# Kernel tuning notes

Hardware: AMD Instinct MI355X
Metric: run time of the kernel (lower is better)

## Reference

```python
import jax, jax.numpy as jnp
import numpy as np

EPS = 1e-12  # matches torch F.normalize eps


def _l2norm(x, axis):
    n = jnp.sqrt(jnp.sum(x * x, axis=axis, keepdims=True))
    return x / jnp.maximum(n, EPS)


def setup_inputs() -> dict:
    key = jax.random.key(0)
    ks = jax.random.split(key, 12)
    B, C, H, W = 64, 2048, 14, 14
    hs, k = 1024, 512

    def xavier(kk, shape):
        fan_out, fan_in = shape[0], shape[1]
        a = float(np.sqrt(6.0 / (fan_in + fan_out)))
        return jax.random.uniform(kk, shape, jnp.float32, -a, a)

    return {
        "img": jax.random.normal(ks[0], (B, C, H, W), jnp.float32),
        "h": jax.random.normal(ks[1], (B, hs), jnp.float32),
        "wc": xavier(ks[2], (k, 1)),
        "bc": xavier(ks[3], (k, 1)),
        "whc": xavier(ks[4], (k, hs)),
        "wci": xavier(ks[5], (1, k)),
        "bci": xavier(ks[6], (1, 1)),
        "ws": xavier(ks[7], (k, C)),
        "bs": xavier(ks[8], (k, 1)),
        "whs": xavier(ks[9], (k, hs)),
        "wsi": xavier(ks[10], (1, k)),
        "bsi": xavier(ks[11], (1, 1)),
    }


def reference(img, h, wc, bc, whc, wci, bci, ws, bs, whs, wsi, bsi):
    B, C, H, W = img.shape
    P = H * W
    x = img.reshape(B, C, P)

    # ---- channel attention ----
    xc = _l2norm(x, axis=2)                      # normalize each channel over spatial
    ic = jnp.mean(xc, axis=2)                    # avgpool over HW -> [B, C]
    # wc [k,1] @ ic[:,None,:] [B,1,C] is a rank-1 outer product -> [B,k,C]
    t = jnp.tanh(wc[None, :, :] * ic[:, None, :] + bc[None, :, :]
                 + jnp.einsum('kh,bh->bk', whc, h)[:, :, None])  # [B,k,C]
    sc = jnp.einsum('k,bkc->bc', wci[0], t) + bci[0, 0]
    ac = jax.nn.softmax(sc, axis=1)              # [B, C]
    xw = x * ac[:, :, None]                      # channel-weighted features [B,C,P]

    # ---- spatial attention ----
    xs = _l2norm(xw, axis=1)                     # normalize each position over channels
    st = jnp.tanh(jnp.einsum('kc,bcp->bkp', ws, xs) + bs[None, :, :]
                  + jnp.einsum('kh,bh->bk', whs, h)[:, :, None])  # [B,k,P]
    ss = jnp.einsum('k,bkp->bp', wsi[0], st) + bsi[0, 0]
    asp = jax.nn.softmax(ss, axis=1)             # [B, P]
    out = xw * asp[:, None, :]                   # [B,C,P]
    return out.reshape(B, C, H, W)
```

## Files before the change

### kernel.cpp

```cpp
#include <hip/hip_runtime.h>

typedef unsigned short u16;
typedef short bf16x8 __attribute__((ext_vector_type(8)));
typedef float f32x4 __attribute__((ext_vector_type(4)));
typedef unsigned short u16x8 __attribute__((ext_vector_type(8)));

#define B_DIM 64
#define C_DIM 2048
#define P_DIM 196
#define K_DIM 512
#define HS_DIM 1024

static __device__ __forceinline__ u16 f2bf(float f) {
    union { float f; unsigned u; } v; v.f = f;
    unsigned r = v.u + 0x7FFF + ((v.u >> 16) & 1);
    return (u16)(r >> 16);
}

static __device__ __forceinline__ float fast_tanh(float a) {
    float e = __expf(2.f * a);
    return 1.f - 2.f / (e + 1.f);
}

__global__ void k1_rowstats(const float* __restrict__ x, float* __restrict__ ic) {
    int row = blockIdx.x * 4 + (threadIdx.x >> 6);
    int l = threadIdx.x & 63;
    const float* r = x + (size_t)row * P_DIM;
    float a0 = r[l], a1 = r[64 + l], a2 = r[128 + l];
    float a3 = (l < 4) ? r[192 + l] : 0.f;
    float s = a0 + a1 + a2 + a3;
    float q = a0 * a0 + a1 * a1 + a2 * a2 + a3 * a3;
    for (int off = 32; off; off >>= 1) { s += __shfl_down(s, off); q += __shfl_down(q, off); }
    if (l == 0) {
        float n = fmaxf(sqrtf(q), 1e-12f);
        ic[row] = s / ((float)P_DIM * n);
    }
}

__global__ __launch_bounds__(256) void k2_hproj(
    const float* __restrict__ h, const float* __restrict__ whc,
    const float* __restrict__ bc, const float* __restrict__ whs,
    const float* __restrict__ bs, float* __restrict__ u, float* __restrict__ v) {
    __shared__ float rc[1024], rs[1024];
    int k = blockIdx.x;
    int t = threadIdx.x, w = t >> 6, l = t & 63;
    for (int i = t; i < 1024; i += 256) {
        rc[i] = whc[(size_t)k * HS_DIM + i];
        rs[i] = whs[(size_t)k * HS_DIM + i];
    }
    __syncthreads();
    float bcv = bc[k], bsv = bs[k];
    for (int bb = 0; bb < 16; ++bb) {
        int b = (w << 4) + bb;
        const float* hr = h + (size_t)b * HS_DIM;
        float su = 0.f, sv = 0.f;
        #pragma unroll
        for (int j = 0; j < 16; ++j) {
            float hv = hr[l + (j << 6)];
            su = fmaf(rc[l + (j << 6)], hv, su);
            sv = fmaf(rs[l + (j << 6)], hv, sv);
        }
        #pragma unroll
        for (int off = 32; off; off >>= 1) { su += __shfl_down(su, off); sv += __shfl_down(sv, off); }
        if (l == 0) { u[b * K_DIM + k] = su + bcv; v[b * K_DIM + k] = sv + bsv; }
    }
}

__global__ void k2b_conv(const float* __restrict__ ws, u16* __restrict__ wsb2) {
    int i = blockIdx.x * 256 + threadIdx.x;
    int lane = i & 63;
    int kb = (i >> 6) & 31;
    int cstep = i >> 11;
    int r = kb * 16 + (lane & 15);
    int c0 = (cstep << 5) + ((lane >> 4) << 3);
    const float* src = ws + (size_t)r * C_DIM + c0;
    float4 f0 = *(const float4*)(src);
    float4 f1 = *(const float4*)(src + 4);
    u16x8 o;
    o[0] = f2bf(f0.x); o[1] = f2bf(f0.y); o[2] = f2bf(f0.z); o[3] = f2bf(f0.w);
    o[4] = f2bf(f1.x); o[5] = f2bf(f1.y); o[6] = f2bf(f1.z); o[7] = f2bf(f1.w);
    *(u16x8*)(wsb2 + (size_t)i * 8) = o;
}

__global__ void k3_sc(const float* __restrict__ ic, const float* __restrict__ u,
                      const float* __restrict__ wc, const float* __restrict__ wci,
                      const float* __restrict__ bci, float* __restrict__ sc) {
    __shared__ float swc[512], swci[512], su[512];
    int b = blockIdx.y;
    int c = blockIdx.x * 256 + threadIdx.x;
    for (int i = threadIdx.x; i < 512; i += 256) {
        swc[i] = wc[i]; swci[i] = wci[i]; su[i] = u[b * 512 + i];
    }
    __syncthreads();
    float icv = ic[(size_t)b * C_DIM + c];
    float s = 0.f;
    #pragma unroll 8
    for (int k = 0; k < 512; k++) {
        float a = fmaf(swc[k], icv, su[k]);
        s = fmaf(swci[k], fast_tanh(a), s);
    }
    sc[(size_t)b * C_DIM + c] = s + bci[0];
}

__global__ void k4_softmax_c(const float* __restrict__ sc, float* __restrict__ ac) {
    int b = blockIdx.x, t = threadIdx.x;
    __shared__ float red[4], red2[4];
    const float* s = sc + (size_t)b * C_DIM;
    float vals[8]; float m = -1e30f;
    #pragma unroll
    for (int i = 0; i < 8; i++) { vals[i] = s[t + i * 256]; m = fmaxf(m, vals[i]); }
    for (int off = 32; off; off >>= 1) m = fmaxf(m, __shfl_xor(m, off));
    if ((t & 63) == 0) red[t >> 6] = m;
    __syncthreads();
    m = fmaxf(fmaxf(red[0], red[1]), fmaxf(red[2], red[3]));
    float sum = 0.f;
    #pragma unroll
    for (int i = 0; i < 8; i++) { vals[i] = __expf(vals[i] - m); sum += vals[i]; }
    for (int off = 32; off; off >>= 1) sum += __shfl_xor(sum, off);
    if ((t & 63) == 0) red2[t >> 6] = sum;
    __syncthreads();
    sum = red2[0] + red2[1] + red2[2] + red2[3];
    float inv = 1.f / sum;
    float* a = ac + (size_t)b * C_DIM;
    #pragma unroll
    for (int i = 0; i < 8; i++) a[t + i * 256] = vals[i] * inv;
}

__global__ __launch_bounds__(256, 2) void k5_gemm(
    const float* __restrict__ x, const u16* __restrict__ wsb2,
    const float* __restrict__ ac, const float* __restrict__ vv,
    const float* __restrict__ wsi, float* __restrict__ ssp) {
    __shared__ __align__(16) u16 lB[2][64 * 32];
    __shared__ float lred[256];
    __shared__ float lcn[64];
    __shared__ float lss[4][64];

    const int p0 = blockIdx.x * 64;
    const int Rb = blockIdx.y * 256;
    const int b  = blockIdx.z;
    const int t = threadIdx.x;
    const int w = t >> 6, l = t & 63;
    const int lr16 = l & 15, lh = l >> 4;
    const int pg = l;
    const int co = w << 3;
    const int pp = p0 + pg;
    const bool pvld = pp < P_DIM;
    const int sBw = (pg >> 1) & 3;

    f32x4 acc[4][4];
    #pragma unroll
    for (int i = 0; i < 4; i++)
        #pragma unroll
        for (int j = 0; j < 4; j++)
            acc[i][j] = (f32x4){0.f, 0.f, 0.f, 0.f};

    float psum = 0.f;
    const float* xcol = x + (size_t)b * (C_DIM * P_DIM) + pp;
    const float* acrow = ac + (size_t)b * C_DIM;
    const bf16x8* abase = (const bf16x8*)wsb2 + ((Rb >> 4) + (w << 2)) * 64 + l;

    float xv[2][8], av[2][8];
    bf16x8 af[4][4];

    auto LOADX = [&](int step, int xs) {
        const int cc = (step << 5) + co;
        #pragma unroll
        for (int j = 0; j < 8; ++j)
            xv[xs][j] = pvld ? xcol[(size_t)(cc + j) * P_DIM] : 0.f;
        float4 a0 = *(const float4*)(acrow + cc);
        float4 a1 = *(const float4*)(acrow + cc + 4);
        av[xs][0] = a0.x; av[xs][1] = a0.y; av[xs][2] = a0.z; av[xs][3] = a0.w;
        av[xs][4] = a1.x; av[xs][5] = a1.y; av[xs][6] = a1.z; av[xs][7] = a1.w;
    };
    auto LOADA = [&](int step, int as_) {
        const bf16x8* p = abase + (size_t)step * 2048;
        #pragma unroll
        for (int mt = 0; mt < 4; ++mt) af[as_][mt] = p[mt * 64];
    };
    auto PROCB = [&](int xs, int bufi) {
        u16x8 pk;
        #pragma unroll
        for (int j = 0; j < 8; ++j) {
            float xw = xv[xs][j] * av[xs][j];
            psum = fmaf(xw, xw, psum);
            pk[j] = f2bf(xw);
        }
        *(u16x8*)&lB[bufi][(pg << 5) + ((w ^ sBw) << 3)] = pk;
    };
    auto RD_B = [&](int bufi, bf16x8* bfr) {
        #pragma unroll
        for (int nt = 0; nt < 4; ++nt) {
            int r = (nt << 4) + lr16;
            int s = (r >> 1) & 3;
            bfr[nt] = *(const bf16x8*)&lB[bufi][(r << 5) + ((lh ^ s) << 3)];
        }
    };
    auto MFMA16 = [&](int as_, const bf16x8* bfr) {
        __builtin_amdgcn_s_setprio(1);
        #pragma unroll
        for (int mt = 0; mt < 4; ++mt)
            #pragma unroll
            for (int nt = 0; nt < 4; ++nt)
                acc[mt][nt] = __builtin_amdgcn_mfma_f32_16x16x32_bf16(
                    af[as_][mt], bfr[nt], acc[mt][nt], 0, 0, 0);
        __builtin_amdgcn_s_setprio(0);
    };

    LOADX(0, 0); LOADA(0, 0);
    LOADX(1, 1); LOADA(1, 1);
    PROCB(0, 0);
    asm volatile("s_waitcnt lgkmcnt(0)" ::: "memory");
    __builtin_amdgcn_s_barrier();

    for (int ii = 0; ii < 15; ++ii) {
        const int base = ii << 2;
        #pragma unroll
        for (int S = 0; S < 4; ++S) {
            bf16x8 bfr[4];
            RD_B(S & 1, bfr);
            LOADX(base + S + 2, S & 1);
            LOADA(base + S + 2, (S + 2) & 3);
            MFMA16(S & 3, bfr);
            PROCB((S + 1) & 1, (S + 1) & 1);
            asm volatile("s_waitcnt lgkmcnt(0)" ::: "memory");
            __builtin_amdgcn_s_barrier();
        }
    }
    #pragma unroll
    for (int S = 0; S < 4; ++S) {
        bf16x8 bfr[4];
        RD_B(S & 1, bfr);
        if (S < 2) { LOADX(62 + S, S & 1); LOADA(62 + S, (S + 2) & 3); }
        MFMA16(S & 3, bfr);
        if (S < 3) PROCB((S + 1) & 1, (S + 1) & 1);
        asm volatile("s_waitcnt lgkmcnt(0)" ::: "memory");
        __builtin_amdgcn_s_barrier();
    }

    lred[t] = psum;
    __syncthreads();
    if (t < 64) {
        float cs = lred[t] + lred[t + 64] + lred[t + 128] + lred[t + 192];
        lcn[t] = fmaxf(sqrtf(cs), 1e-12f);
    }
    __syncthreads();

    float ssv[4] = {0.f, 0.f, 0.f, 0.f};
    #pragma unroll
    for (int mt = 0; mt < 4; ++mt) {
        int rl = (w << 6) + (mt << 4) + (lh << 2);
        #pragma unroll
        for (int j = 0; j < 4; ++j) {
            int r = Rb + rl + j;
            float wsiv = wsi[r];
            float vb = vv[b * K_DIM + r];
            #pragma unroll
            for (int nt = 0; nt < 4; ++nt) {
                float cn = lcn[(nt << 4) + lr16];
                float a = acc[mt][nt][j] / cn + vb;
                ssv[nt] = fmaf(wsiv, fast_tanh(a), ssv[nt]);
            }
        }
    }
    #pragma unroll
    for (int nt = 0; nt < 4; ++nt) {
        ssv[nt] += __shfl_xor(ssv[nt], 16);
        ssv[nt] += __shfl_xor(ssv[nt], 32);
    }
    if (lh == 0) {
        #pragma unroll
        for (int nt = 0; nt < 4; ++nt) lss[w][(nt << 4) + lr16] = ssv[nt];
    }
    __syncthreads();
    if (t < 64) {
        float s = lss[0][t] + lss[1][t] + lss[2][t] + lss[3][t];
        ssp[((blockIdx.y << 6) + b) * 256 + p0 + t] = s;
    }
}

__global__ void k6_softmax_p(const float* __restrict__ ssp, const float* __restrict__ bsi,
                             float* __restrict__ asp) {
    int b = blockIdx.x, t = threadIdx.x;
    __shared__ float red[4], red2[4];
    float val = -1e30f;
    if (t < P_DIM) val = ssp[b * 256 + t] + ssp[(64 + b) * 256 + t] + bsi[0];
    float m = val;
    for (int off = 32; off; off >>= 1) m = fmaxf(m, __shfl_xor(m, off));
    if ((t & 63) == 0) red[t >> 6] = m;
    __syncthreads();
    m = fmaxf(fmaxf(red[0], red[1]), fmaxf(red[2], red[3]));
    float e = (t < P_DIM) ? __expf(val - m) : 0.f;
    float sum = e;
    for (int off = 32; off; off >>= 1) sum += __shfl_xor(sum, off);
    if ((t & 63) == 0) red2[t >> 6] = sum;
    __syncthreads();
    sum = red2[0] + red2[1] + red2[2] + red2[3];
    if (t < P_DIM) asp[b * P_DIM + t] = e / sum;
}

__global__ void k7_out(const float* __restrict__ x, const float* __restrict__ ac,
                       const float* __restrict__ asp, float* __restrict__ out) {
    int idx = blockIdx.x * 256 + threadIdx.x;
    int row = idx / 49;
    int pq = idx - row * 49;
    int b = row >> 11;
    float a = ac[row];
    float4 xv = ((const float4*)x)[idx];
    float4 pv = *(const float4*)&asp[b * P_DIM + pq * 4];
    float4 o;
    o.x = xv.x * a * pv.x;
    o.y = xv.y * a * pv.y;
    o.z = xv.z * a * pv.z;
    o.w = xv.w * a * pv.w;
    ((float4*)out)[idx] = o;
}

extern "C" void kernel_launch(void* const* d_in, const int* in_sizes, int n_in,
                              void* d_out, int out_size, void* d_ws, size_t ws_size,
                              hipStream_t stream) {
    const float* img = (const float*)d_in[0];
    const float* h   = (const float*)d_in[1];
    const float* wc  = (const float*)d_in[2];
    const float* bc  = (const float*)d_in[3];
    const float* whc = (const float*)d_in[4];
    const float* wci = (const float*)d_in[5];
    const float* bci = (const float*)d_in[6];
    const float* ws  = (const float*)d_in[7];
    const float* bs  = (const float*)d_in[8];
    const float* whs = (const float*)d_in[9];
    const float* wsi = (const float*)d_in[10];
    const float* bsi = (const float*)d_in[11];
    float* out = (float*)d_out;

    char* wsp = (char*)d_ws;
    float* ic  = (float*)(wsp);
    float* u   = (float*)(wsp + 524288);
    float* v   = (float*)(wsp + 655360);
    float* sc  = (float*)(wsp + 786432);
    float* ac  = (float*)(wsp + 1310720);
    float* ssp = (float*)(wsp + 1835008);
    float* asp = (float*)(wsp + 1966080);
    u16*   wsb2 = (u16*)(wsp + 2097152);

    k1_rowstats<<<dim3(32768), dim3(256), 0, stream>>>(img, ic);
    k2_hproj<<<dim3(512), dim3(256), 0, stream>>>(h, whc, bc, whs, bs, u, v);
    k2b_conv<<<dim3(512), dim3(256), 0, stream>>>(ws, wsb2);
    k3_sc<<<dim3(8, 64), dim3(256), 0, stream>>>(ic, u, wc, wci, bci, sc);
    k4_softmax_c<<<dim3(64), dim3(256), 0, stream>>>(sc, ac);
    k5_gemm<<<dim3(4, 2, 64), dim3(256), 0, stream>>>(img, wsb2, ac, v, wsi, ssp);
    k6_softmax_p<<<dim3(64), dim3(256), 0, stream>>>(ssp, bsi, asp);
    k7_out<<<dim3(25088), dim3(256), 0, stream>>>(img, ac, asp, out);
}
```

Before: 332.1 us.

## Precompute channel-weighted features in bf16 with column norms via atomics

Adds a kernel that multiplies the input by the channel attention weights once, stores the result as bf16, and accumulates per-position squared norms with atomicAdd into a buffer that the channel softmax kernel zeroes. The GEMM kernel then reads the bf16 tensor instead of the fp32 input plus attention weights. The output kernel also reads it, which halves the bytes each consumer pulls and removes the in-GEMM norm reduction. In exchange it adds an extra write pass with scalar 2-byte stores and strided 2-byte gathers in the GEMM. The final output is now computed from bf16-rounded values, which reduces its precision.

```diff
diff --git a/kernel.cpp b/kernel.cpp
--- a/kernel.cpp
+++ b/kernel.cpp
@@ -15,6 +15,11 @@
     union { float f; unsigned u; } v; v.f = f;
     unsigned r = v.u + 0x7FFF + ((v.u >> 16) & 1);
     return (u16)(r >> 16);
+}
+
+static __device__ __forceinline__ float bf2f(u16 b) {
+    union { unsigned u; float f; } v; v.u = ((unsigned)b) << 16;
+    return v.f;
 }
 
 static __device__ __forceinline__ float fast_tanh(float a) {
@@ -102,9 +107,11 @@
     sc[(size_t)b * C_DIM + c] = s + bci[0];
 }
 
-__global__ void k4_softmax_c(const float* __restrict__ sc, float* __restrict__ ac) {
+__global__ void k4_softmax_c(const float* __restrict__ sc, float* __restrict__ ac,
+                             float* __restrict__ cnsq) {
     int b = blockIdx.x, t = threadIdx.x;
     __shared__ float red[4], red2[4];
+    if (t < P_DIM) cnsq[b * P_DIM + t] = 0.f;
     const float* s = sc + (size_t)b * C_DIM;
     float vals[8]; float m = -1e30f;
     #pragma unroll
@@ -126,13 +133,43 @@
     for (int i = 0; i < 8; i++) a[t + i * 256] = vals[i] * inv;
 }
 
+__global__ __launch_bounds__(256) void k_xw(
+    const float* __restrict__ x, const float* __restrict__ ac,
+    u16* __restrict__ xw, float* __restrict__ cnsq) {
+    __shared__ float psq[4][200];
+    int b = blockIdx.y;
+    int c0 = blockIdx.x * 128 + (threadIdx.x >> 6) * 32;
+    int w = threadIdx.x >> 6, l = threadIdx.x & 63;
+    const float* xb = x + ((size_t)b * C_DIM + c0) * P_DIM;
+    u16* xwb = xw + ((size_t)b * C_DIM + c0) * P_DIM;
+    const float* acb = ac + (size_t)b * C_DIM + c0;
+    float q0 = 0.f, q1 = 0.f, q2 = 0.f, q3 = 0.f;
+    for (int i = 0; i < 32; ++i) {
+        const float* r = xb + (size_t)i * P_DIM;
+        float a = acb[i];
+        float v0 = r[l] * a, v1 = r[64 + l] * a, v2 = r[128 + l] * a;
+        float v3 = (l < 4) ? r[192 + l] * a : 0.f;
+        q0 = fmaf(v0, v0, q0); q1 = fmaf(v1, v1, q1);
+        q2 = fmaf(v2, v2, q2); q3 = fmaf(v3, v3, q3);
+        u16* o = xwb + (size_t)i * P_DIM;
+        o[l] = f2bf(v0); o[64 + l] = f2bf(v1); o[128 + l] = f2bf(v2);
+        if (l < 4) o[192 + l] = f2bf(v3);
+    }
+    psq[w][l] = q0; psq[w][64 + l] = q1; psq[w][128 + l] = q2;
+    if (l < 4) psq[w][192 + l] = q3;
+    __syncthreads();
+    int t = threadIdx.x;
+    if (t < P_DIM) {
+        float s = psq[0][t] + psq[1][t] + psq[2][t] + psq[3][t];
+        atomicAdd(cnsq + b * P_DIM + t, s);
+    }
+}
+
 __global__ __launch_bounds__(256, 2) void k5_gemm(
-    const float* __restrict__ x, const u16* __restrict__ wsb2,
-    const float* __restrict__ ac, const float* __restrict__ vv,
+    const u16* __restrict__ xw, const u16* __restrict__ wsb2,
+    const float* __restrict__ cnsq, const float* __restrict__ vv,
     const float* __restrict__ wsi, float* __restrict__ ssp) {
     __shared__ __align__(16) u16 lB[2][64 * 32];
-    __shared__ float lred[256];
-    __shared__ float lcn[64];
     __shared__ float lss[4][64];
 
     const int p0 = blockIdx.x * 64;
@@ -154,23 +191,17 @@
         for (int j = 0; j < 4; j++)
             acc[i][j] = (f32x4){0.f, 0.f, 0.f, 0.f};
 
-    float psum = 0.f;
-    const float* xcol = x + (size_t)b * (C_DIM * P_DIM) + pp;
-    const float* acrow = ac + (size_t)b * C_DIM;
+    const u16* xcol = xw + (size_t)b * (C_DIM * P_DIM) + pp;
     const bf16x8* abase = (const bf16x8*)wsb2 + ((Rb >> 4) + (w << 2)) * 64 + l;
 
-    float xv[2][8], av[2][8];
+    u16 xv[2][8];
     bf16x8 af[4][4];
 
     auto LOADX = [&](int step, int xs) {
         const int cc = (step << 5) + co;
         #pragma unroll
         for (int j = 0; j < 8; ++j)
-            xv[xs][j] = pvld ? xcol[(size_t)(cc + j) * P_DIM] : 0.f;
-        float4 a0 = *(const float4*)(acrow + cc);
-        float4 a1 = *(const float4*)(acrow + cc + 4);
-        av[xs][0] = a0.x; av[xs][1] = a0.y; av[xs][2] = a0.z; av[xs][3] = a0.w;
-        av[xs][4] = a1.x; av[xs][5] = a1.y; av[xs][6] = a1.z; av[xs][7] = a1.w;
+            xv[xs][j] = pvld ? xcol[(size_t)(cc + j) * P_DIM] : (u16)0;
     };
     auto LOADA = [&](int step, int as_) {
         const bf16x8* p = abase + (size_t)step * 2048;
@@ -180,11 +211,7 @@
     auto PROCB = [&](int xs, int bufi) {
         u16x8 pk;
         #pragma unroll
-        for (int j = 0; j < 8; ++j) {
-            float xw = xv[xs][j] * av[xs][j];
-            psum = fmaf(xw, xw, psum);
-            pk[j] = f2bf(xw);
-        }
+        for (int j = 0; j < 8; ++j) pk[j] = xv[xs][j];
         *(u16x8*)&lB[bufi][(pg << 5) + ((w ^ sBw) << 3)] = pk;
     };
     auto RD_B = [&](int bufi, bf16x8* bfr) {
@@ -237,13 +264,12 @@
         __builtin_amdgcn_s_barrier();
     }
 
-    lred[t] = psum;
-    __syncthreads();
-    if (t < 64) {
-        float cs = lred[t] + lred[t + 64] + lred[t + 128] + lred[t + 192];
-        lcn[t] = fmaxf(sqrtf(cs), 1e-12f);
-    }
-    __syncthreads();
+    float cns[4];
+    #pragma unroll
+    for (int nt = 0; nt < 4; ++nt) {
+        int col = p0 + (nt << 4) + lr16;
+        cns[nt] = (col < P_DIM) ? fmaxf(sqrtf(cnsq[b * P_DIM + col]), 1e-12f) : 1.f;
+    }
 
     float ssv[4] = {0.f, 0.f, 0.f, 0.f};
     #pragma unroll
@@ -256,8 +282,7 @@
             float vb = vv[b * K_DIM + r];
             #pragma unroll
             for (int nt = 0; nt < 4; ++nt) {
-                float cn = lcn[(nt << 4) + lr16];
-                float a = acc[mt][nt][j] / cn + vb;
+                float a = acc[mt][nt][j] / cns[nt] + vb;
                 ssv[nt] = fmaf(wsiv, fast_tanh(a), ssv[nt]);
             }
         }
@@ -298,20 +323,19 @@
     if (t < P_DIM) asp[b * P_DIM + t] = e / sum;
 }
 
-__global__ void k7_out(const float* __restrict__ x, const float* __restrict__ ac,
-                       const float* __restrict__ asp, float* __restrict__ out) {
+__global__ void k7_out(const u16* __restrict__ xw, const float* __restrict__ asp,
+                       float* __restrict__ out) {
     int idx = blockIdx.x * 256 + threadIdx.x;
     int row = idx / 49;
     int pq = idx - row * 49;
     int b = row >> 11;
-    float a = ac[row];
-    float4 xv = ((const float4*)x)[idx];
+    uint2 xv = *(const uint2*)(xw + (size_t)row * P_DIM + pq * 4);
     float4 pv = *(const float4*)&asp[b * P_DIM + pq * 4];
     float4 o;
-    o.x = xv.x * a * pv.x;
-    o.y = xv.y * a * pv.y;
-    o.z = xv.z * a * pv.z;
-    o.w = xv.w * a * pv.w;
+    o.x = bf2f((u16)(xv.x & 0xffff)) * pv.x;
+    o.y = bf2f((u16)(xv.x >> 16))    * pv.y;
+    o.z = bf2f((u16)(xv.y & 0xffff)) * pv.z;
+    o.w = bf2f((u16)(xv.y >> 16))    * pv.w;
     ((float4*)out)[idx] = o;
 }
 
@@ -333,21 +357,24 @@
     float* out = (float*)d_out;
 
     char* wsp = (char*)d_ws;
-    float* ic  = (float*)(wsp);
-    float* u   = (float*)(wsp + 524288);
-    float* v   = (float*)(wsp + 655360);
-    float* sc  = (float*)(wsp + 786432);
-    float* ac  = (float*)(wsp + 1310720);
-    float* ssp = (float*)(wsp + 1835008);
-    float* asp = (float*)(wsp + 1966080);
-    u16*   wsb2 = (u16*)(wsp + 2097152);
+    float* ic   = (float*)(wsp);
+    float* u    = (float*)(wsp + 0x080000);
+    float* v    = (float*)(wsp + 0x0A0000);
+    float* sc   = (float*)(wsp + 0x0C0000);
+    float* ac   = (float*)(wsp + 0x140000);
+    float* ssp  = (float*)(wsp + 0x1C0000);
+    float* asp  = (float*)(wsp + 0x1E0000);
+    float* cnsq = (float*)(wsp + 0x1F0000);
+    u16*   wsb2 = (u16*)  (wsp + 0x200000);
+    u16*   xw   = (u16*)  (wsp + 0x400000);
 
     k1_rowstats<<<dim3(32768), dim3(256), 0, stream>>>(img, ic);
     k2_hproj<<<dim3(512), dim3(256), 0, stream>>>(h, whc, bc, whs, bs, u, v);
     k2b_conv<<<dim3(512), dim3(256), 0, stream>>>(ws, wsb2);
     k3_sc<<<dim3(8, 64), dim3(256), 0, stream>>>(ic, u, wc, wci, bci, sc);
-    k4_softmax_c<<<dim3(64), dim3(256), 0, stream>>>(sc, ac);
-    k5_gemm<<<dim3(4, 2, 64), dim3(256), 0, stream>>>(img, wsb2, ac, v, wsi, ssp);
+    k4_softmax_c<<<dim3(64), dim3(256), 0, stream>>>(sc, ac, cnsq);
+    k_xw<<<dim3(16, 64), dim3(256), 0, stream>>>(img, ac, xw, cnsq);
+    k5_gemm<<<dim3(4, 2, 64), dim3(256), 0, stream>>>(xw, wsb2, cnsq, v, wsi, ssp);
     k6_softmax_p<<<dim3(64), dim3(256), 0, stream>>>(ssp, bsi, asp);
-    k7_out<<<dim3(25088), dim3(256), 0, stream>>>(img, ac, asp, out);
-}
+    k7_out<<<dim3(25088), dim3(256), 0, stream>>>(xw, asp, out);
+}
```

Result: slower. 385.6 us (+16.1%).
